# Kernel tuning notes

Measured on AMD Instinct MI355X. Metric: run time of the kernel, lower is better.

The kernel has to match this reference:

```python
import jax, jax.numpy as jnp
import numpy as np

B = 524288   # batch rows
K = 8        # number of BooleanClassifiers
I = 64       # n_inputs
H = 32       # n_hidden
SCALE = 1.0  # LinearNetwork.scale (default [1.0])


def setup_inputs() -> dict:
    key = jax.random.key(0)
    k_x, k_w1, k_b1, k_w2, k_b2 = jax.random.split(key, 5)
    return {
        "x": jax.random.normal(k_x, (B, I), dtype=jnp.float32),
        "W1": jax.random.normal(k_w1, (K, H, I), dtype=jnp.float32) * 0.1,
        "b1": jax.random.normal(k_b1, (K, H), dtype=jnp.float32) * 0.1,
        "W2": jax.random.normal(k_w2, (K, H), dtype=jnp.float32) * 0.1,
        "b2": jax.random.normal(k_b2, (K,), dtype=jnp.float32) * 0.1,
        "bias": jnp.zeros((K,), dtype=jnp.float32),  # unused in training-mode forward
    }


def reference(x, W1, b1, W2, b2, bias):
    # Loop of K tiny Linear-Tanh-Linear-Tanh classifiers, fused as batched GEMMs.
    # h: [B, K, H]
    h = jnp.tanh(jnp.einsum("bi,khi->bkh", x, W1) + b1)
    # per-classifier scalar output, concatenated along dim=1 -> [B, K]
    out = jnp.tanh(jnp.einsum("bkh,kh->bk", h, W2) + b2)
    out = out * SCALE                   # LinearNetwork scale
    out = (out + 1.0) * 0.5 * SCALE     # LinearWithTanh training branch
    return out
```

## Files before the change

kernel.cpp:

```cpp
#include <hip/hip_runtime.h>
#include <hip/hip_bf16.h>

typedef __attribute__((ext_vector_type(8))) short short8;
typedef __attribute__((ext_vector_type(4))) float f32x4;

constexpr int B_ROWS   = 524288;
constexpr int ROWTILES = B_ROWS / 64;

__device__ __forceinline__ float fast_tanh(float x) {
  float e = __builtin_amdgcn_exp2f(x * 2.8853900817779268f);
  return 1.0f - 2.0f * __builtin_amdgcn_rcpf(e + 1.0f);
}

__device__ __forceinline__ short bf16_rne(float f) {
  union { float f; unsigned u; } v; v.f = f;
  unsigned u = v.u + 0x7FFFu + ((v.u >> 16) & 1u);
  return (short)(u >> 16);
}

__device__ __forceinline__ short8 pack8(f32x4 a, f32x4 b) {
  short8 f;
  f[0] = bf16_rne(a[0]); f[1] = bf16_rne(a[1]);
  f[2] = bf16_rne(a[2]); f[3] = bf16_rne(a[3]);
  f[4] = bf16_rne(b[0]); f[5] = bf16_rne(b[1]);
  f[6] = bf16_rne(b[2]); f[7] = bf16_rne(b[3]);
  return f;
}

__global__ __launch_bounds__(256, 4) void fused_mlp8(
    const float* __restrict__ x, const float* __restrict__ W1,
    const float* __restrict__ b1, const float* __restrict__ W2,
    const float* __restrict__ b2, float* __restrict__ out) {

  __shared__ short8 xch[512];

  const int tid  = threadIdx.x;
  const int wave = tid >> 6;
  const int lane = tid & 63;
  const int m16  = lane & 15;
  const int q    = lane >> 4;

  short8 w1f[4][2];
#pragma unroll
  for (int mt = 0; mt < 4; ++mt) {
    const int n = (wave * 4 + mt) * 16 + m16;
#pragma unroll
    for (int ks = 0; ks < 2; ++ks) {
      const float* p = W1 + n * 64 + ks * 32 + q * 8;
      w1f[mt][ks] = pack8(*(const f32x4*)p, *(const f32x4*)(p + 4));
    }
  }

  f32x4 b1v[4], w2v[4];
#pragma unroll
  for (int mt = 0; mt < 4; ++mt) {
    const int n0 = (wave * 4 + mt) * 16 + q * 4;
    b1v[mt] = *(const f32x4*)(b1 + n0);
    w2v[mt] = *(const f32x4*)(W2 + n0);
  }
  const float b2v[2] = { b2[wave * 2], b2[wave * 2 + 1] };

  for (int it = blockIdx.x; it < ROWTILES; it += gridDim.x) {
    const long base = (long)it * 64;

#pragma unroll
    for (int cc = 0; cc < 2; ++cc) {
      const int c   = tid * 2 + cc;
      const int tt  = c >> 7;
      const int ks  = (c >> 6) & 1;
      const int cl  = c & 63;
      const int row = tt * 16 + (cl & 15);
      const int col = ks * 32 + (cl >> 4) * 8;
      const float* p = x + (base + row) * 64 + col;
      xch[c] = pack8(*(const f32x4*)p, *(const f32x4*)(p + 4));
    }
    __syncthreads();

#pragma unroll
    for (int tt = 0; tt < 4; ++tt) {
      const short8 xf0 = xch[(tt * 2 + 0) * 64 + lane];
      const short8 xf1 = xch[(tt * 2 + 1) * 64 + lane];

      f32x4 acc[4];
#pragma unroll
      for (int mt = 0; mt < 4; ++mt) {
        f32x4 z = { 0.f, 0.f, 0.f, 0.f };
        z = __builtin_amdgcn_mfma_f32_16x16x32_bf16(w1f[mt][0], xf0, z, 0, 0, 0);
        z = __builtin_amdgcn_mfma_f32_16x16x32_bf16(w1f[mt][1], xf1, z, 0, 0, 0);
        acc[mt] = z;
      }

      float o0 = 0.f, o1 = 0.f;
#pragma unroll
      for (int j = 0; j < 2; ++j) {
        float S = 0.f;
#pragma unroll
        for (int t = 0; t < 2; ++t) {
          const int mt = j * 2 + t;
#pragma unroll
          for (int r = 0; r < 4; ++r)
            S += fast_tanh(acc[mt][r] + b1v[mt][r]) * w2v[mt][r];
        }
        S += __shfl_xor(S, 16);
        S += __shfl_xor(S, 32);
        const float o = 0.5f * fast_tanh(S + b2v[j]) + 0.5f;
        if (j == 0) o0 = o; else o1 = o;
      }

      if (q == 0) {
        float2 st; st.x = o0; st.y = o1;
        *(float2*)(out + (base + tt * 16 + m16) * 8 + wave * 2) = st;
      }
    }
    __syncthreads();
  }
}

extern "C" void kernel_launch(void* const* d_in, const int* in_sizes, int n_in,
                              void* d_out, int out_size, void* d_ws, size_t ws_size,
                              hipStream_t stream) {
  const float* x  = (const float*)d_in[0];
  const float* W1 = (const float*)d_in[1];
  const float* b1 = (const float*)d_in[2];
  const float* W2 = (const float*)d_in[3];
  const float* b2 = (const float*)d_in[4];
  float* out = (float*)d_out;
  fused_mlp8<<<1024, 256, 0, stream>>>(x, W1, b1, W2, b2, out);
}
```

Measured before the change: 216.4 us.

## Prefetch next x tile into registers, fold tanh constants, double grid size

Loads the next row tile of x into registers while the current tile is being computed, so global-load latency overlaps the MFMA and tanh work. Algebraically folds the tanh constants: bias is prescaled by 2*log2(e), W2 is prescaled by -2, and sum(W2) is folded into the output bias. This cuts the per-element work to one FMA, one exp2, one rcp and one FMA. The grid goes from 1024 to 2048 blocks. The price is extra registers for the prefetch buffer, which may reduce occupancy under the launch bounds.

```diff
diff --git a/kernel.cpp b/kernel.cpp
--- a/kernel.cpp
+++ b/kernel.cpp
@@ -6,11 +6,8 @@
 
 constexpr int B_ROWS   = 524288;
 constexpr int ROWTILES = B_ROWS / 64;
-
-__device__ __forceinline__ float fast_tanh(float x) {
-  float e = __builtin_amdgcn_exp2f(x * 2.8853900817779268f);
-  return 1.0f - 2.0f * __builtin_amdgcn_rcpf(e + 1.0f);
-}
+constexpr int GRID     = 2048;
+constexpr float L2E2   = 2.8853900817779268f;
 
 __device__ __forceinline__ short bf16_rne(float f) {
   union { float f; unsigned u; } v; v.f = f;
@@ -51,31 +48,63 @@
     }
   }
 
-  f32x4 b1v[4], w2v[4];
+  f32x4 kb1[4], w2m[4];
+  float sw2[2] = {0.f, 0.f};
 #pragma unroll
   for (int mt = 0; mt < 4; ++mt) {
     const int n0 = (wave * 4 + mt) * 16 + q * 4;
-    b1v[mt] = *(const f32x4*)(b1 + n0);
-    w2v[mt] = *(const f32x4*)(W2 + n0);
+    const f32x4 b1x = *(const f32x4*)(b1 + n0);
+    const f32x4 w2x = *(const f32x4*)(W2 + n0);
+#pragma unroll
+    for (int r = 0; r < 4; ++r) {
+      kb1[mt][r] = L2E2 * b1x[r];
+      w2m[mt][r] = -2.0f * w2x[r];
+      sw2[mt >> 1] += w2x[r];
+    }
   }
-  const float b2v[2] = { b2[wave * 2], b2[wave * 2 + 1] };
+  float KSb[2];
+#pragma unroll
+  for (int j = 0; j < 2; ++j) {
+    float s = sw2[j];
+    s += __shfl_xor(s, 16);
+    s += __shfl_xor(s, 32);
+    KSb[j] = L2E2 * (s + b2[wave * 2 + j]);
+  }
 
-  for (int it = blockIdx.x; it < ROWTILES; it += gridDim.x) {
-    const long base = (long)it * 64;
-
+  f32x4 pf[2][2];
+  {
+    const long base = (long)blockIdx.x * 64;
 #pragma unroll
     for (int cc = 0; cc < 2; ++cc) {
-      const int c   = tid * 2 + cc;
-      const int tt  = c >> 7;
-      const int ks  = (c >> 6) & 1;
-      const int cl  = c & 63;
-      const int row = tt * 16 + (cl & 15);
-      const int col = ks * 32 + (cl >> 4) * 8;
+      const int c   = tid + cc * 256;
+      const int row = (c >> 7) * 16 + (c & 15);
+      const int col = ((c >> 6) & 1) * 32 + ((c & 63) >> 4) * 8;
       const float* p = x + (base + row) * 64 + col;
-      xch[c] = pack8(*(const f32x4*)p, *(const f32x4*)(p + 4));
+      pf[cc][0] = *(const f32x4*)p;
+      pf[cc][1] = *(const f32x4*)(p + 4);
     }
+  }
+
+  for (int it = blockIdx.x; it < ROWTILES; it += GRID) {
+    xch[tid]       = pack8(pf[0][0], pf[0][1]);
+    xch[tid + 256] = pack8(pf[1][0], pf[1][1]);
     __syncthreads();
 
+    const int itn = it + GRID;
+    if (itn < ROWTILES) {
+      const long nbase = (long)itn * 64;
+#pragma unroll
+      for (int cc = 0; cc < 2; ++cc) {
+        const int c   = tid + cc * 256;
+        const int row = (c >> 7) * 16 + (c & 15);
+        const int col = ((c >> 6) & 1) * 32 + ((c & 63) >> 4) * 8;
+        const float* p = x + (nbase + row) * 64 + col;
+        pf[cc][0] = *(const f32x4*)p;
+        pf[cc][1] = *(const f32x4*)(p + 4);
+      }
+    }
+
+    const long base = (long)it * 64;
 #pragma unroll
     for (int tt = 0; tt < 4; ++tt) {
       const short8 xf0 = xch[(tt * 2 + 0) * 64 + lane];
@@ -93,17 +122,22 @@
       float o0 = 0.f, o1 = 0.f;
 #pragma unroll
       for (int j = 0; j < 2; ++j) {
-        float S = 0.f;
+        float P = 0.f;
 #pragma unroll
         for (int t = 0; t < 2; ++t) {
           const int mt = j * 2 + t;
 #pragma unroll
-          for (int r = 0; r < 4; ++r)
-            S += fast_tanh(acc[mt][r] + b1v[mt][r]) * w2v[mt][r];
+          for (int r = 0; r < 4; ++r) {
+            const float e = __builtin_amdgcn_exp2f(
+                __builtin_fmaf(acc[mt][r], L2E2, kb1[mt][r]));
+            P = __builtin_fmaf(w2m[mt][r], __builtin_amdgcn_rcpf(e + 1.0f), P);
+          }
         }
-        S += __shfl_xor(S, 16);
-        S += __shfl_xor(S, 32);
-        const float o = 0.5f * fast_tanh(S + b2v[j]) + 0.5f;
+        P += __shfl_xor(P, 16);
+        P += __shfl_xor(P, 32);
+        const float arg = __builtin_fmaf(P, L2E2, KSb[j]);
+        const float o = 1.0f - __builtin_amdgcn_rcpf(
+            __builtin_amdgcn_exp2f(arg) + 1.0f);
         if (j == 0) o0 = o; else o1 = o;
       }
 
@@ -125,5 +159,5 @@
   const float* W2 = (const float*)d_in[3];
   const float* b2 = (const float*)d_in[4];
   float* out = (float*)d_out;
-  fused_mlp8<<<1024, 256, 0, stream>>>(x, W1, b1, W2, b2, out);
+  fused_mlp8<<<GRID, 256, 0, stream>>>(x, W1, b1, W2, b2, out);
 }
```

Measured after the change: 216.2 us. Within noise of the previous version (-0.1%).
